# Optimization experiments

Hardware: AMD Instinct MI355X
Metric: run time of the kernel (lower is better)

Reference implementation:

```python
import jax, jax.numpy as jnp
import numpy as np
from jax import lax

H = 64  # hidden size of both LSTM layers


def _lstm(x, W_ih, W_hh, b_ih, b_hh):
    """Single-layer batch-first LSTM (torch gate order i,f,g,o).
    x: [B,S,F]; returns (all_h [B,S,H], last_h [B,H])."""
    B, S, _ = x.shape
    # Precompute input projections for all timesteps at once: [B,S,4H]
    xp = jnp.einsum('bsf,gf->bsg', x, W_ih) + b_ih + b_hh

    def step(carry, xt):  # xt: [B,4H]
        h, c = carry
        z = xt + h @ W_hh.T
        i, f, g, o = jnp.split(z, 4, axis=-1)
        i = jax.nn.sigmoid(i)
        f = jax.nn.sigmoid(f)
        g = jnp.tanh(g)
        o = jax.nn.sigmoid(o)
        c = f * c + i * g
        h = o * jnp.tanh(c)
        return (h, c), h

    h0 = jnp.zeros((B, H), x.dtype)
    c0 = jnp.zeros((B, H), x.dtype)
    (h_last, _), hs = lax.scan(step, (h0, c0), jnp.swapaxes(xp, 0, 1))
    return jnp.swapaxes(hs, 0, 1), h_last


def setup_inputs() -> dict:
    key = jax.random.key(0)
    ks = jax.random.split(key, 14)
    B, S, F, OUT = 4096, 512, 1, 24
    s = 1.0 / np.sqrt(H)  # torch default uniform bound ~ 1/sqrt(hidden)
    r = lambda k, shape: jax.random.uniform(k, shape, jnp.float32, -s, s)
    return {
        'x': jax.random.normal(ks[0], (B, S, F), jnp.float32),
        'W_ih1': r(ks[1], (4 * H, F)),
        'W_hh1': r(ks[2], (4 * H, H)),
        'b_ih1': r(ks[3], (4 * H,)),
        'b_hh1': r(ks[4], (4 * H,)),
        'W_ih2': r(ks[5], (4 * H, H)),
        'W_hh2': r(ks[6], (4 * H, H)),
        'b_ih2': r(ks[7], (4 * H,)),
        'b_hh2': r(ks[8], (4 * H,)),
        'W_d1': r(ks[9], (32, H)),
        'b_d1': r(ks[10], (32,)),
        'W_d2': r(ks[11], (OUT, 32)),
        'b_d2': r(ks[12], (OUT,)),
    }


def reference(x, W_ih1, W_hh1, b_ih1, b_hh1, W_ih2, W_hh2, b_ih2, b_hh2,
              W_d1, b_d1, W_d2, b_d2):
    h1, _ = _lstm(x, W_ih1, W_hh1, b_ih1, b_hh1)          # [B,S,64]
    # dropout1 is identity in eval mode
    _, h_last = _lstm(h1, W_ih2, W_hh2, b_ih2, b_hh2)     # [B,64]
    # dropout2 is identity in eval mode
    y = jax.nn.relu(h_last @ W_d1.T + b_d1)                # [B,32]
    return y @ W_d2.T + b_d2                               # [B,24]
```

## Files before the change

kernel.cpp:

```cpp
#include <hip/hip_runtime.h>


typedef __attribute__((ext_vector_type(8))) short bf16x8;
typedef __attribute__((ext_vector_type(4))) float floatx4;

#define SEQ 512
#define HID 64
#define LOG2E 1.4426950408889634f

__device__ inline floatx4 MFMA(bf16x8 a, bf16x8 b, floatx4 c) {
    return __builtin_amdgcn_mfma_f32_16x16x32_bf16(a, b, c, 0, 0, 0);
}
__device__ inline short f2bf(float f) {
    __bf16 b = (__bf16)f;
    return __builtin_bit_cast(short, b);
}
__device__ inline float exp2_fast(float x) {
#if __has_builtin(__builtin_amdgcn_exp2f)
    return __builtin_amdgcn_exp2f(x);
#else
    return __expf(x * 0.6931471805599453f);
#endif
}
__device__ inline float rcp_fast(float x) { return __builtin_amdgcn_rcpf(x); }

__device__ inline float lstm_gate(float zi, float zf, float zg, float zo, float& c) {
    float ei = exp2_fast(zi);
    float ef = exp2_fast(zf);
    float eg = exp2_fast(zg);
    float eo = exp2_fast(zo);
    float P  = (1.0f + ei) * (1.0f + eg);
    float F  = 1.0f + ef;
    float num = c * P + (1.0f - eg) * F;
    c = num * rcp_fast(P * F);
    float ec = exp2_fast(fminf(c * (-2.0f * LOG2E), 40.0f));
    return (1.0f - ec) * rcp_fast((1.0f + eo) * (1.0f + ec));
}

__global__ __launch_bounds__(512, 2) void lstm_fused(
    const float* __restrict__ x,
    const float* __restrict__ Wih1, const float* __restrict__ Whh1,
    const float* __restrict__ bih1, const float* __restrict__ bhh1,
    const float* __restrict__ Wih2, const float* __restrict__ Whh2,
    const float* __restrict__ bih2, const float* __restrict__ bhh2,
    const float* __restrict__ Wd1,  const float* __restrict__ bd1,
    const float* __restrict__ Wd2,  const float* __restrict__ bd2,
    float* __restrict__ out)
{
    const int tid  = threadIdx.x;
    const int wave = tid >> 6;
    const int ct   = wave & 3;
    const int is2  = wave >> 2;
    const int lane = tid & 63;
    const int l15  = lane & 15;
    const int quad = lane >> 4;
    const int b0   = blockIdx.x * 16;

    __shared__ __align__(16) float x_s[16][516];
    __shared__ __align__(16) short h1_s[2][16][72];
    __shared__ __align__(16) short h2_s[2][16][72];
    __shared__ float y1_s[16][32];

    {
        const int row = tid >> 5;
        const int c0  = (tid & 31) * 16;
        const float4* src = reinterpret_cast<const float4*>(x + (size_t)(b0 + row) * SEQ + c0);
        float4* dst = reinterpret_cast<float4*>(&x_s[row][c0]);
        #pragma unroll
        for (int j = 0; j < 4; ++j) dst[j] = src[j];
    }
    for (int i = tid; i < 2 * 16 * 72; i += 512) {
        (&h1_s[0][0][0])[i] = 0;
        (&h2_s[0][0][0])[i] = 0;
    }

    bf16x8 Wf[4][4];
    float wxc[4], bcs[4];
    #pragma unroll
    for (int g = 0; g < 4; ++g) {
        const float sc = (g == 2) ? (-2.0f * LOG2E) : (-LOG2E);
        const int col = g * 64 + ct * 16 + l15;
        if (!is2) {
            wxc[g] = Wih1[col] * sc;
            bcs[g] = (bih1[col] + bhh1[col]) * sc;
        } else {
            wxc[g] = 0.0f;
            bcs[g] = (bih2[col] + bhh2[col]) * sc;
        }
        #pragma unroll
        for (int kt = 0; kt < 2; ++kt) {
            const int koff = kt * 32 + quad * 8;
            union { short s[8]; bf16x8 v; } u0, u1;
            #pragma unroll
            for (int j = 0; j < 8; ++j) {
                if (!is2) {
                    u0.s[j] = f2bf(Whh1[col * HID + koff + j] * sc);
                    u1.s[j] = 0;
                } else {
                    u0.s[j] = f2bf(Wih2[col * HID + koff + j] * sc);
                    u1.s[j] = f2bf(Whh2[col * HID + koff + j] * sc);
                }
            }
            Wf[kt][g] = u0.v;
            Wf[2 + kt][g] = u1.v;
        }
    }

    const int hcol = ct * 16 + l15;
    float cst[4] = {0, 0, 0, 0};

    #pragma unroll 2
    for (int t = 0; t < SEQ; ++t) {
        const int pr1 = (t + 1) & 1;
        const int pr2 = t & 1;
        __syncthreads();
        if (!is2) {
            const bf16x8 A1a = *reinterpret_cast<const bf16x8*>(&h1_s[pr1][l15][quad * 8]);
            const bf16x8 A1b = *reinterpret_cast<const bf16x8*>(&h1_s[pr1][l15][32 + quad * 8]);
            floatx4 z[4];
            #pragma unroll
            for (int g = 0; g < 4; ++g)
                #pragma unroll
                for (int r = 0; r < 4; ++r)
                    z[g][r] = x_s[quad * 4 + r][t] * wxc[g] + bcs[g];
            #pragma unroll
            for (int g = 0; g < 4; ++g) {
                z[g] = MFMA(A1a, Wf[0][g], z[g]);
                z[g] = MFMA(A1b, Wf[1][g], z[g]);
            }
            #pragma unroll
            for (int r = 0; r < 4; ++r) {
                float h1v = lstm_gate(z[0][r], z[1][r], z[2][r], z[3][r], cst[r]);
                h1_s[pr2][quad * 4 + r][hcol] = f2bf(h1v);
            }
        } else {
            const bf16x8 A1a = *reinterpret_cast<const bf16x8*>(&h1_s[pr1][l15][quad * 8]);
            const bf16x8 A1b = *reinterpret_cast<const bf16x8*>(&h1_s[pr1][l15][32 + quad * 8]);
            const bf16x8 A2a = *reinterpret_cast<const bf16x8*>(&h2_s[pr2][l15][quad * 8]);
            const bf16x8 A2b = *reinterpret_cast<const bf16x8*>(&h2_s[pr2][l15][32 + quad * 8]);
            floatx4 z[4];
            #pragma unroll
            for (int g = 0; g < 4; ++g)
                z[g] = floatx4{bcs[g], bcs[g], bcs[g], bcs[g]};
            #pragma unroll
            for (int g = 0; g < 4; ++g) {
                z[g] = MFMA(A1a, Wf[0][g], z[g]);
                z[g] = MFMA(A1b, Wf[1][g], z[g]);
                z[g] = MFMA(A2a, Wf[2][g], z[g]);
                z[g] = MFMA(A2b, Wf[3][g], z[g]);
            }
            const float m2 = (t == 0) ? 0.0f : 1.0f;
            #pragma unroll
            for (int r = 0; r < 4; ++r) {
                float cc = cst[r];
                float h2v = lstm_gate(z[0][r], z[1][r], z[2][r], z[3][r], cc) * m2;
                cst[r] = cc * m2;
                h2_s[pr1][quad * 4 + r][hcol] = f2bf(h2v);
            }
        }
    }

    __syncthreads();
    if (is2) {
        const bf16x8 A1a = *reinterpret_cast<const bf16x8*>(&h1_s[1][l15][quad * 8]);
        const bf16x8 A1b = *reinterpret_cast<const bf16x8*>(&h1_s[1][l15][32 + quad * 8]);
        const bf16x8 A2a = *reinterpret_cast<const bf16x8*>(&h2_s[0][l15][quad * 8]);
        const bf16x8 A2b = *reinterpret_cast<const bf16x8*>(&h2_s[0][l15][32 + quad * 8]);
        floatx4 z[4];
        #pragma unroll
        for (int g = 0; g < 4; ++g) {
            z[g] = floatx4{bcs[g], bcs[g], bcs[g], bcs[g]};
            z[g] = MFMA(A1a, Wf[0][g], z[g]);
            z[g] = MFMA(A1b, Wf[1][g], z[g]);
            z[g] = MFMA(A2a, Wf[2][g], z[g]);
            z[g] = MFMA(A2b, Wf[3][g], z[g]);
        }
        float* h2f = &x_s[0][0];
        #pragma unroll
        for (int r = 0; r < 4; ++r) {
            float cc = cst[r];
            float h2v = lstm_gate(z[0][r], z[1][r], z[2][r], z[3][r], cc);
            h2f[(quad * 4 + r) * HID + hcol] = h2v;
        }
    }
    __syncthreads();

    const float* h2f = &x_s[0][0];
    for (int idx = tid; idx < 16 * 32; idx += 512) {
        const int b = idx >> 5, o = idx & 31;
        float acc = bd1[o];
        #pragma unroll 8
        for (int k = 0; k < HID; ++k) acc += h2f[b * HID + k] * Wd1[o * HID + k];
        y1_s[b][o] = fmaxf(acc, 0.0f);
    }
    __syncthreads();
    for (int idx = tid; idx < 16 * 24; idx += 512) {
        const int b = idx / 24, o = idx - b * 24;
        float acc = bd2[o];
        #pragma unroll 8
        for (int k = 0; k < 32; ++k) acc += y1_s[b][k] * Wd2[o * 32 + k];
        out[(size_t)(b0 + b) * 24 + o] = acc;
    }
}

extern "C" void kernel_launch(void* const* d_in, const int* in_sizes, int n_in,
                              void* d_out, int out_size, void* d_ws, size_t ws_size,
                              hipStream_t stream) {
    const float* x    = (const float*)d_in[0];
    const float* Wih1 = (const float*)d_in[1];
    const float* Whh1 = (const float*)d_in[2];
    const float* bih1 = (const float*)d_in[3];
    const float* bhh1 = (const float*)d_in[4];
    const float* Wih2 = (const float*)d_in[5];
    const float* Whh2 = (const float*)d_in[6];
    const float* bih2 = (const float*)d_in[7];
    const float* bhh2 = (const float*)d_in[8];
    const float* Wd1  = (const float*)d_in[9];
    const float* bd1  = (const float*)d_in[10];
    const float* Wd2  = (const float*)d_in[11];
    const float* bd2  = (const float*)d_in[12];
    float* out = (float*)d_out;

    lstm_fused<<<256, 512, 0, stream>>>(x, Wih1, Whh1, bih1, bhh1,
                                        Wih2, Whh2, bih2, bhh2,
                                        Wd1, bd1, Wd2, bd2, out);
}
```

Before: 466.2 us.

## Double block to 1024 threads and split LSTM gate rows across wave pairs

Launches 16 waves per block instead of 8. Each (layer, column-tile) pair of waves repeats the same MFMA work, but each wave evaluates the transcendental-heavy gate math and cell-state update for only two of the four accumulator rows. The aim is to shorten the per-timestep critical path of elementwise gate work and add latency hiding on each CU. In exchange, matrix work is duplicated and register pressure rises. The `__launch_bounds__(1024, 4)` hint may also restrict registers enough to cause spills.

```diff
diff --git a/kernel.cpp b/kernel.cpp
--- a/kernel.cpp
+++ b/kernel.cpp
@@ -37,7 +37,7 @@
     return (1.0f - ec) * rcp_fast((1.0f + eo) * (1.0f + ec));
 }
 
-__global__ __launch_bounds__(512, 2) void lstm_fused(
+__global__ __launch_bounds__(1024, 4) void lstm_fused(
     const float* __restrict__ x,
     const float* __restrict__ Wih1, const float* __restrict__ Whh1,
     const float* __restrict__ bih1, const float* __restrict__ bhh1,
@@ -48,9 +48,10 @@
     float* __restrict__ out)
 {
     const int tid  = threadIdx.x;
-    const int wave = tid >> 6;
-    const int ct   = wave & 3;
-    const int is2  = wave >> 2;
+    const int wid  = tid >> 6;
+    const int ct   = wid & 3;
+    const int is2  = (wid >> 2) & 1;
+    const int rh   = wid >> 3;
     const int lane = tid & 63;
     const int l15  = lane & 15;
     const int quad = lane >> 4;
@@ -62,14 +63,14 @@
     __shared__ float y1_s[16][32];
 
     {
-        const int row = tid >> 5;
-        const int c0  = (tid & 31) * 16;
+        const int row = wid;
+        const int c0  = lane * 8;
         const float4* src = reinterpret_cast<const float4*>(x + (size_t)(b0 + row) * SEQ + c0);
         float4* dst = reinterpret_cast<float4*>(&x_s[row][c0]);
-        #pragma unroll
-        for (int j = 0; j < 4; ++j) dst[j] = src[j];
-    }
-    for (int i = tid; i < 2 * 16 * 72; i += 512) {
+        dst[0] = src[0];
+        dst[1] = src[1];
+    }
+    for (int i = tid; i < 2 * 16 * 72; i += 1024) {
         (&h1_s[0][0][0])[i] = 0;
         (&h2_s[0][0][0])[i] = 0;
     }
@@ -106,8 +107,18 @@
         }
     }
 
-    const int hcol = ct * 16 + l15;
-    float cst[4] = {0, 0, 0, 0};
+    const int hcol  = ct * 16 + l15;
+    const int rbase = quad * 4 + rh * 2;
+    float cst[2] = {0, 0};
+
+#define L1_ROW(r, cr) { \
+        float h1v = lstm_gate(z[0][r], z[1][r], z[2][r], z[3][r], cr); \
+        h1_s[pr2][quad * 4 + (r)][hcol] = f2bf(h1v); }
+#define L2_ROW(r, cr) { \
+        float cc = cr; \
+        float h2v = lstm_gate(z[0][r], z[1][r], z[2][r], z[3][r], cc) * m2; \
+        cr = cc * m2; \
+        h2_s[pr1][quad * 4 + (r)][hcol] = f2bf(h2v); }
 
     #pragma unroll 2
     for (int t = 0; t < SEQ; ++t) {
@@ -120,19 +131,31 @@
             floatx4 z[4];
             #pragma unroll
             for (int g = 0; g < 4; ++g)
-                #pragma unroll
-                for (int r = 0; r < 4; ++r)
-                    z[g][r] = x_s[quad * 4 + r][t] * wxc[g] + bcs[g];
+                z[g] = floatx4{bcs[g], bcs[g], bcs[g], bcs[g]};
+            {
+                const float xa = x_s[rbase][t];
+                const float xb = x_s[rbase + 1][t];
+                if (rh == 0) {
+                    #pragma unroll
+                    for (int g = 0; g < 4; ++g) {
+                        z[g][0] += xa * wxc[g];
+                        z[g][1] += xb * wxc[g];
+                    }
+                } else {
+                    #pragma unroll
+                    for (int g = 0; g < 4; ++g) {
+                        z[g][2] += xa * wxc[g];
+                        z[g][3] += xb * wxc[g];
+                    }
+                }
+            }
             #pragma unroll
             for (int g = 0; g < 4; ++g) {
                 z[g] = MFMA(A1a, Wf[0][g], z[g]);
                 z[g] = MFMA(A1b, Wf[1][g], z[g]);
             }
-            #pragma unroll
-            for (int r = 0; r < 4; ++r) {
-                float h1v = lstm_gate(z[0][r], z[1][r], z[2][r], z[3][r], cst[r]);
-                h1_s[pr2][quad * 4 + r][hcol] = f2bf(h1v);
-            }
+            if (rh == 0) { L1_ROW(0, cst[0]); L1_ROW(1, cst[1]); }
+            else         { L1_ROW(2, cst[0]); L1_ROW(3, cst[1]); }
         } else {
             const bf16x8 A1a = *reinterpret_cast<const bf16x8*>(&h1_s[pr1][l15][quad * 8]);
             const bf16x8 A1b = *reinterpret_cast<const bf16x8*>(&h1_s[pr1][l15][32 + quad * 8]);
@@ -150,13 +173,8 @@
                 z[g] = MFMA(A2b, Wf[3][g], z[g]);
             }
             const float m2 = (t == 0) ? 0.0f : 1.0f;
-            #pragma unroll
-            for (int r = 0; r < 4; ++r) {
-                float cc = cst[r];
-                float h2v = lstm_gate(z[0][r], z[1][r], z[2][r], z[3][r], cc) * m2;
-                cst[r] = cc * m2;
-                h2_s[pr1][quad * 4 + r][hcol] = f2bf(h2v);
-            }
+            if (rh == 0) { L2_ROW(0, cst[0]); L2_ROW(1, cst[1]); }
+            else         { L2_ROW(2, cst[0]); L2_ROW(3, cst[1]); }
         }
     }
 
@@ -176,17 +194,17 @@
             z[g] = MFMA(A2b, Wf[3][g], z[g]);
         }
         float* h2f = &x_s[0][0];
-        #pragma unroll
-        for (int r = 0; r < 4; ++r) {
-            float cc = cst[r];
-            float h2v = lstm_gate(z[0][r], z[1][r], z[2][r], z[3][r], cc);
-            h2f[(quad * 4 + r) * HID + hcol] = h2v;
-        }
+#define DR_ROW(r, cr) { \
+            float cc = cr; \
+            float h2v = lstm_gate(z[0][r], z[1][r], z[2][r], z[3][r], cc); \
+            h2f[(quad * 4 + (r)) * HID + hcol] = h2v; }
+        if (rh == 0) { DR_ROW(0, cst[0]); DR_ROW(1, cst[1]); }
+        else         { DR_ROW(2, cst[0]); DR_ROW(3, cst[1]); }
     }
     __syncthreads();
 
     const float* h2f = &x_s[0][0];
-    for (int idx = tid; idx < 16 * 32; idx += 512) {
+    for (int idx = tid; idx < 16 * 32; idx += 1024) {
         const int b = idx >> 5, o = idx & 31;
         float acc = bd1[o];
         #pragma unroll 8
@@ -194,7 +212,7 @@
         y1_s[b][o] = fmaxf(acc, 0.0f);
     }
     __syncthreads();
-    for (int idx = tid; idx < 16 * 24; idx += 512) {
+    for (int idx = tid; idx < 16 * 24; idx += 1024) {
         const int b = idx / 24, o = idx - b * 24;
         float acc = bd2[o];
         #pragma unroll 8
@@ -221,7 +239,7 @@
     const float* bd2  = (const float*)d_in[12];
     float* out = (float*)d_out;
 
-    lstm_fused<<<256, 512, 0, stream>>>(x, Wih1, Whh1, bih1, bhh1,
-                                        Wih2, Whh2, bih2, bhh2,
-                                        Wd1, bd1, Wd2, bd2, out);
-}
+    lstm_fused<<<256, 1024, 0, stream>>>(x, Wih1, Whh1, bih1, bhh1,
+                                         Wih2, Whh2, bih2, bhh2,
+                                         Wd1, bd1, Wd2, bd2, out);
+}
```

After: 812.0 us. 1.74x slower.

## Replace per-step block barriers with LDS progress-counter flags between LSTM layers

Applied to the files above, without the earlier changes.

Drops the per-timestep __syncthreads. Layer-1 and layer-2 waves now run in separate loops and coordinate through shared-memory progress counters polled with volatile loads. Layer 1 may now run up to two steps ahead of layer 2, so the h1 buffer grows to four slots. A large unused padding array in shared memory is added, apparently to cap occupancy at one block per CU. The spin-waiting costs issue slots, and the visibility ordering relies on __threadfence_block and volatile accesses.

```diff
diff --git a/kernel.cpp b/kernel.cpp
--- a/kernel.cpp
+++ b/kernel.cpp
@@ -23,6 +23,10 @@
 #endif
 }
 __device__ inline float rcp_fast(float x) { return __builtin_amdgcn_rcpf(x); }
+
+__device__ inline int min4v(volatile int* p) {
+    return min(min(p[0], p[1]), min(p[2], p[3]));
+}
 
 __device__ inline float lstm_gate(float zi, float zf, float zg, float zo, float& c) {
     float ei = exp2_fast(zi);
@@ -37,7 +41,8 @@
     return (1.0f - ec) * rcp_fast((1.0f + eo) * (1.0f + ec));
 }
 
-__global__ __launch_bounds__(512, 2) void lstm_fused(
+__global__ __launch_bounds__(512, 2)
+void lstm_fused(
     const float* __restrict__ x,
     const float* __restrict__ Wih1, const float* __restrict__ Whh1,
     const float* __restrict__ bih1, const float* __restrict__ bhh1,
@@ -48,18 +53,22 @@
     float* __restrict__ out)
 {
     const int tid  = threadIdx.x;
-    const int wave = tid >> 6;
-    const int ct   = wave & 3;
-    const int is2  = wave >> 2;
+    const int wid  = tid >> 6;
+    const int ct   = wid & 3;
+    const int is2  = wid >> 2;
     const int lane = tid & 63;
     const int l15  = lane & 15;
     const int quad = lane >> 4;
     const int b0   = blockIdx.x * 16;
 
     __shared__ __align__(16) float x_s[16][516];
-    __shared__ __align__(16) short h1_s[2][16][72];
+    __shared__ __align__(16) short h1_s[4][16][72];
     __shared__ __align__(16) short h2_s[2][16][72];
     __shared__ float y1_s[16][32];
+    __shared__ __align__(16) int prog1[4];
+    __shared__ __align__(16) int prog2[4];
+    __shared__ float pad_s[8448];
+    if (blockIdx.x == 0xFFFFFFFFu) ((volatile float*)pad_s)[tid] = 1.0f;
 
     {
         const int row = tid >> 5;
@@ -69,54 +78,49 @@
         #pragma unroll
         for (int j = 0; j < 4; ++j) dst[j] = src[j];
     }
-    for (int i = tid; i < 2 * 16 * 72; i += 512) {
-        (&h1_s[0][0][0])[i] = 0;
-        (&h2_s[0][0][0])[i] = 0;
-    }
-
-    bf16x8 Wf[4][4];
-    float wxc[4], bcs[4];
-    #pragma unroll
-    for (int g = 0; g < 4; ++g) {
-        const float sc = (g == 2) ? (-2.0f * LOG2E) : (-LOG2E);
-        const int col = g * 64 + ct * 16 + l15;
-        if (!is2) {
+    for (int i = tid; i < 4 * 16 * 72; i += 512) (&h1_s[0][0][0])[i] = 0;
+    for (int i = tid; i < 2 * 16 * 72; i += 512) (&h2_s[0][0][0])[i] = 0;
+    if (tid < 4) { prog1[tid] = 0; prog2[tid] = 0; }
+
+    const int hcol = ct * 16 + l15;
+    volatile int* vp1 = prog1;
+    volatile int* vp2 = prog2;
+
+    __syncthreads();
+
+    if (!is2) {
+        bf16x8 Wf[2][4];
+        float wxc[4], bcs[4];
+        #pragma unroll
+        for (int g = 0; g < 4; ++g) {
+            const float sc = (g == 2) ? (-2.0f * LOG2E) : (-LOG2E);
+            const int col = g * 64 + hcol;
             wxc[g] = Wih1[col] * sc;
             bcs[g] = (bih1[col] + bhh1[col]) * sc;
-        } else {
-            wxc[g] = 0.0f;
-            bcs[g] = (bih2[col] + bhh2[col]) * sc;
-        }
-        #pragma unroll
-        for (int kt = 0; kt < 2; ++kt) {
-            const int koff = kt * 32 + quad * 8;
-            union { short s[8]; bf16x8 v; } u0, u1;
-            #pragma unroll
-            for (int j = 0; j < 8; ++j) {
-                if (!is2) {
-                    u0.s[j] = f2bf(Whh1[col * HID + koff + j] * sc);
-                    u1.s[j] = 0;
-                } else {
-                    u0.s[j] = f2bf(Wih2[col * HID + koff + j] * sc);
-                    u1.s[j] = f2bf(Whh2[col * HID + koff + j] * sc);
-                }
-            }
-            Wf[kt][g] = u0.v;
-            Wf[2 + kt][g] = u1.v;
-        }
-    }
-
-    const int hcol = ct * 16 + l15;
-    float cst[4] = {0, 0, 0, 0};
-
-    #pragma unroll 2
-    for (int t = 0; t < SEQ; ++t) {
-        const int pr1 = (t + 1) & 1;
-        const int pr2 = t & 1;
-        __syncthreads();
-        if (!is2) {
-            const bf16x8 A1a = *reinterpret_cast<const bf16x8*>(&h1_s[pr1][l15][quad * 8]);
-            const bf16x8 A1b = *reinterpret_cast<const bf16x8*>(&h1_s[pr1][l15][32 + quad * 8]);
+            #pragma unroll
+            for (int kt = 0; kt < 2; ++kt) {
+                const int koff = kt * 32 + quad * 8;
+                union { short s[8]; bf16x8 v; } u;
+                #pragma unroll
+                for (int j = 0; j < 8; ++j)
+                    u.s[j] = f2bf(Whh1[col * HID + koff + j] * sc);
+                Wf[kt][g] = u.v;
+            }
+        }
+        float cst[4] = {0, 0, 0, 0};
+        int m1 = 0, m2 = 0;
+        for (int t = 0; t < SEQ; ++t) {
+            const int rs = (t - 1) & 3;
+            const int ws = t & 3;
+            if (m1 < t || m2 < t - 2) {
+                do {
+                    m1 = min4v(vp1);
+                    m2 = min4v(vp2);
+                } while (m1 < t || m2 < t - 2);
+            }
+            asm volatile("" ::: "memory");
+            const bf16x8 A1a = *reinterpret_cast<const bf16x8*>(&h1_s[rs][l15][quad * 8]);
+            const bf16x8 A1b = *reinterpret_cast<const bf16x8*>(&h1_s[rs][l15][32 + quad * 8]);
             floatx4 z[4];
             #pragma unroll
             for (int g = 0; g < 4; ++g)
@@ -124,63 +128,102 @@
                 for (int r = 0; r < 4; ++r)
                     z[g][r] = x_s[quad * 4 + r][t] * wxc[g] + bcs[g];
             #pragma unroll
-            for (int g = 0; g < 4; ++g) {
-                z[g] = MFMA(A1a, Wf[0][g], z[g]);
-                z[g] = MFMA(A1b, Wf[1][g], z[g]);
-            }
+            for (int g = 0; g < 4; ++g) z[g] = MFMA(A1a, Wf[0][g], z[g]);
+            #pragma unroll
+            for (int g = 0; g < 4; ++g) z[g] = MFMA(A1b, Wf[1][g], z[g]);
             #pragma unroll
             for (int r = 0; r < 4; ++r) {
-                float h1v = lstm_gate(z[0][r], z[1][r], z[2][r], z[3][r], cst[r]);
-                h1_s[pr2][quad * 4 + r][hcol] = f2bf(h1v);
-            }
-        } else {
-            const bf16x8 A1a = *reinterpret_cast<const bf16x8*>(&h1_s[pr1][l15][quad * 8]);
-            const bf16x8 A1b = *reinterpret_cast<const bf16x8*>(&h1_s[pr1][l15][32 + quad * 8]);
-            const bf16x8 A2a = *reinterpret_cast<const bf16x8*>(&h2_s[pr2][l15][quad * 8]);
-            const bf16x8 A2b = *reinterpret_cast<const bf16x8*>(&h2_s[pr2][l15][32 + quad * 8]);
+                float hv = lstm_gate(z[0][r], z[1][r], z[2][r], z[3][r], cst[r]);
+                h1_s[ws][quad * 4 + r][hcol] = f2bf(hv);
+            }
+            __threadfence_block();
+            if (lane == 0) vp1[ct] = t + 1;
+        }
+    } else {
+        bf16x8 Wf[4][4];
+        float bcs[4];
+        #pragma unroll
+        for (int g = 0; g < 4; ++g) {
+            const float sc = (g == 2) ? (-2.0f * LOG2E) : (-LOG2E);
+            const int col = g * 64 + hcol;
+            bcs[g] = (bih2[col] + bhh2[col]) * sc;
+            #pragma unroll
+            for (int kt = 0; kt < 2; ++kt) {
+                const int koff = kt * 32 + quad * 8;
+                union { short s[8]; bf16x8 v; } u0, u1;
+                #pragma unroll
+                for (int j = 0; j < 8; ++j) {
+                    u0.s[j] = f2bf(Wih2[col * HID + koff + j] * sc);
+                    u1.s[j] = f2bf(Whh2[col * HID + koff + j] * sc);
+                }
+                Wf[kt][g] = u0.v;
+                Wf[2 + kt][g] = u1.v;
+            }
+        }
+        float cst[4] = {0, 0, 0, 0};
+        int m1 = 0, m2 = 0;
+        for (int t = 0; t < SEQ; ++t) {
+            const int rs = (t - 1) & 3;
+            if (m1 < t || m2 < t) {
+                do {
+                    m1 = min4v(vp1);
+                    m2 = min4v(vp2);
+                } while (m1 < t || m2 < t);
+            }
+            asm volatile("" ::: "memory");
+            const bf16x8 A1a = *reinterpret_cast<const bf16x8*>(&h1_s[rs][l15][quad * 8]);
+            const bf16x8 A1b = *reinterpret_cast<const bf16x8*>(&h1_s[rs][l15][32 + quad * 8]);
+            const bf16x8 A2a = *reinterpret_cast<const bf16x8*>(&h2_s[t & 1][l15][quad * 8]);
+            const bf16x8 A2b = *reinterpret_cast<const bf16x8*>(&h2_s[t & 1][l15][32 + quad * 8]);
             floatx4 z[4];
             #pragma unroll
             for (int g = 0; g < 4; ++g)
                 z[g] = floatx4{bcs[g], bcs[g], bcs[g], bcs[g]};
             #pragma unroll
+            for (int g = 0; g < 4; ++g) z[g] = MFMA(A1a, Wf[0][g], z[g]);
+            #pragma unroll
+            for (int g = 0; g < 4; ++g) z[g] = MFMA(A1b, Wf[1][g], z[g]);
+            #pragma unroll
+            for (int g = 0; g < 4; ++g) z[g] = MFMA(A2a, Wf[2][g], z[g]);
+            #pragma unroll
+            for (int g = 0; g < 4; ++g) z[g] = MFMA(A2b, Wf[3][g], z[g]);
+            const float m2f = (t == 0) ? 0.0f : 1.0f;
+            #pragma unroll
+            for (int r = 0; r < 4; ++r) {
+                float cc = cst[r];
+                float hv = lstm_gate(z[0][r], z[1][r], z[2][r], z[3][r], cc) * m2f;
+                cst[r] = cc * m2f;
+                h2_s[(t + 1) & 1][quad * 4 + r][hcol] = f2bf(hv);
+            }
+            __threadfence_block();
+            if (lane == 0) vp2[ct] = t + 1;
+        }
+        {
+            int m1 = 0, m2 = 0;
+            do {
+                m1 = min4v(vp1);
+                m2 = min4v(vp2);
+            } while (m1 < SEQ || m2 < SEQ);
+            asm volatile("" ::: "memory");
+            const bf16x8 A1a = *reinterpret_cast<const bf16x8*>(&h1_s[(SEQ - 1) & 3][l15][quad * 8]);
+            const bf16x8 A1b = *reinterpret_cast<const bf16x8*>(&h1_s[(SEQ - 1) & 3][l15][32 + quad * 8]);
+            const bf16x8 A2a = *reinterpret_cast<const bf16x8*>(&h2_s[SEQ & 1][l15][quad * 8]);
+            const bf16x8 A2b = *reinterpret_cast<const bf16x8*>(&h2_s[SEQ & 1][l15][32 + quad * 8]);
+            floatx4 z[4];
+            #pragma unroll
             for (int g = 0; g < 4; ++g) {
+                z[g] = floatx4{bcs[g], bcs[g], bcs[g], bcs[g]};
                 z[g] = MFMA(A1a, Wf[0][g], z[g]);
                 z[g] = MFMA(A1b, Wf[1][g], z[g]);
                 z[g] = MFMA(A2a, Wf[2][g], z[g]);
                 z[g] = MFMA(A2b, Wf[3][g], z[g]);
             }
-            const float m2 = (t == 0) ? 0.0f : 1.0f;
+            float* h2f = &x_s[0][0];
             #pragma unroll
             for (int r = 0; r < 4; ++r) {
                 float cc = cst[r];
-                float h2v = lstm_gate(z[0][r], z[1][r], z[2][r], z[3][r], cc) * m2;
-                cst[r] = cc * m2;
-                h2_s[pr1][quad * 4 + r][hcol] = f2bf(h2v);
-            }
-        }
-    }
-
-    __syncthreads();
-    if (is2) {
-        const bf16x8 A1a = *reinterpret_cast<const bf16x8*>(&h1_s[1][l15][quad * 8]);
-        const bf16x8 A1b = *reinterpret_cast<const bf16x8*>(&h1_s[1][l15][32 + quad * 8]);
-        const bf16x8 A2a = *reinterpret_cast<const bf16x8*>(&h2_s[0][l15][quad * 8]);
-        const bf16x8 A2b = *reinterpret_cast<const bf16x8*>(&h2_s[0][l15][32 + quad * 8]);
-        floatx4 z[4];
-        #pragma unroll
-        for (int g = 0; g < 4; ++g) {
-            z[g] = floatx4{bcs[g], bcs[g], bcs[g], bcs[g]};
-            z[g] = MFMA(A1a, Wf[0][g], z[g]);
-            z[g] = MFMA(A1b, Wf[1][g], z[g]);
-            z[g] = MFMA(A2a, Wf[2][g], z[g]);
-            z[g] = MFMA(A2b, Wf[3][g], z[g]);
-        }
-        float* h2f = &x_s[0][0];
-        #pragma unroll
-        for (int r = 0; r < 4; ++r) {
-            float cc = cst[r];
-            float h2v = lstm_gate(z[0][r], z[1][r], z[2][r], z[3][r], cc);
-            h2f[(quad * 4 + r) * HID + hcol] = h2v;
+                h2f[(quad * 4 + r) * HID + hcol] = lstm_gate(z[0][r], z[1][r], z[2][r], z[3][r], cc);
+            }
         }
     }
     __syncthreads();
```

Measured after the change: 589.8 us. 26.5% more time.
